# Kernel tuning notes

Measured on AMD Instinct MI355X. Metric: run time of the kernel, lower is better.

Reference implementation:

```python
import jax, jax.numpy as jnp
import numpy as np

P = 64        # patch size
NATOMS = 256  # dictionary atoms
N = 262144    # signal length
K = 262081    # npatches = N - P + 1 (stride-1 sliding patches)
M = 512       # measurement rows of A


def setup_inputs() -> dict:
    key = jax.random.key(0)
    k0, k1, k2, k3, k4, k5, k6 = jax.random.split(key, 7)
    d = jax.random.normal(k0, (1, P, NATOMS), jnp.float32) * 0.1
    x = jax.random.normal(k1, (NATOMS, K), jnp.float32) * 0.1
    ss = jnp.zeros((N, 1), jnp.float32)  # only its shape is used
    vb = (jax.random.uniform(k2, (N, 1)) > 0.05).astype(jnp.float32)
    # stride-1 sliding-window patch indices: column k covers [k, k+P)
    patches = (jnp.arange(K, dtype=jnp.int32)[None, :]
               + jnp.arange(P, dtype=jnp.int32)[:, None])  # [P, K]
    # npp = number of patches covering each signal sample
    npp = jnp.zeros((N, 1), jnp.float32).at[patches.reshape(-1), 0].add(1.0)
    sRef = jax.random.normal(k3, (N, 1), jnp.float32)
    A = jax.random.normal(k4, (M, N), jnp.float32) * 0.01
    Tarr = jax.random.normal(k5, (M, 1), jnp.float32)
    meanY = jnp.float32(0.1)
    ds = jax.random.normal(k6, (N, 1), jnp.float32)
    lam2 = jnp.float32(0.5)
    return {"d": d, "x": x, "ss": ss, "vb": vb, "patches": patches,
            "npp": npp, "sRef": sRef, "A": A, "Tarr": Tarr,
            "meanY": meanY, "ds": ds, "lam2": lam2, "npatches": K}


def reference(d, x, ss, vb, patches, npp, sRef, A, Tarr, meanY, ds, lam2, npatches):
    # ss_b[p, k] = (D @ X)[p, k] + meanY  -> per-patch reconstructions
    ss_b = jnp.squeeze(d) @ x + meanY                      # [P, K]
    # vectorized scatter-add replacing the torch loop over npatches
    ss_p_sum = jnp.zeros_like(ss).at[patches.reshape(-1), 0].add(ss_b.reshape(-1))  # [N,1]
    ss_f = (lam2 * ds + ss_p_sum) / (lam2 + npp)           # [N,1]
    ss_masked = ss_f * vb                                  # [N,1]
    Tref = A @ (ss_masked + sRef)                          # [M,1]
    return jnp.mean((Tref - Tarr) ** 2)
```

## Files before the change

### kernel.cpp

```cpp
#include <hip/hip_runtime.h>


namespace {
constexpr int kP = 64;
constexpr int kA = 256;
constexpr int kN = 262144;
constexpr int kK = 262081;
constexpr int kM = 512;

constexpr int CB = 256;
constexpr int OPT = 16;
constexpr int NB = CB * OPT;
constexpr int NCHUNK = kN / NB;
constexpr int NSPLIT = 16;
constexpr int APS = kA / NSPLIT;
constexpr int XS4 = 1088;
constexpr int DPF = 80;
constexpr int GV_CH = 8;

__device__ __forceinline__ int swz(int l4) { return l4 ^ ((l4 >> 3) & 7); }

__device__ __forceinline__ float f4c(const float4& v, int i) {
  switch (i & 3) {
    case 0: return v.x;
    case 1: return v.y;
    case 2: return v.z;
    default: return v.w;
  }
}

__device__ __forceinline__ void gload_lds16(const void* g, void* l) {
  __builtin_amdgcn_global_load_lds(
      (const __attribute__((address_space(1))) unsigned int*)g,
      (__attribute__((address_space(3))) unsigned int*)l, 16, 0, 0);
}

__device__ __forceinline__ void stage(const float* __restrict__ x, float4* buf,
                                      int a, int n0, int tid) {
  const int SA = (a + 1) & 3;
  const int g4base = (a * kK + n0 - 63 - SA) >> 2;
  const int g4max = (kA / 4) * kK - 1;
  const float4* __restrict__ x4 = (const float4*)x;
  const int wav = tid >> 6, lane = tid & 63;
  const int sl = lane ^ ((lane >> 3) & 7);
#pragma unroll
  for (int r = 0; r < 4; ++r) {
    const int s = r * 4 + wav;
    int g4 = g4base + s * 64 + sl;
    g4 = g4 < 0 ? 0 : (g4 > g4max ? g4max : g4);
    gload_lds16(x4 + g4, buf + s * 64);
  }
  if (tid < 20) {
    int g4 = g4base + 1024 + (tid ^ ((tid >> 3) & 7));
    g4 = g4 < 0 ? 0 : (g4 > g4max ? g4max : g4);
    gload_lds16(x4 + g4, buf + 1024);
  }
}

__device__ __forceinline__ void compute_atom(const float4* __restrict__ xs4,
                                             const float* __restrict__ dpf,
                                             int al, float* __restrict__ acc) {
  const int t4 = (int)threadIdx.x * 4;
  const float4* __restrict__ dp4 = (const float4*)(dpf + al * DPF);
  float4 w[5];
#pragma unroll
  for (int q = 0; q < 4; ++q) w[q] = xs4[swz(t4 + q)];
#pragma unroll
  for (int c = 0; c < 17; ++c) {
    w[(c + 4) % 5] = xs4[swz(t4 + c + 4)];
    float4 D = dp4[c];
#pragma unroll
    for (int i = 0; i < 4; ++i) {
      float coef = f4c(D, i);
#pragma unroll
      for (int j = 0; j < OPT; ++j) {
        int off = i + j;
        acc[j] = fmaf(coef, f4c(w[(c + (off >> 2)) % 5], off & 3), acc[j]);
      }
    }
  }
}

__global__ __launch_bounds__(CB, 4) void conv_kernel(const float* __restrict__ d,
                                                     const float* __restrict__ x,
                                                     float* __restrict__ part) {
  __shared__ float4 xsA[XS4];
  __shared__ float4 xsB[XS4];
  __shared__ float dpf[APS * DPF];
  const int n0 = blockIdx.x * NB;
  const int a0 = blockIdx.y * APS;
  const int tid = threadIdx.x;

  for (int idx = tid; idx < APS * DPF; idx += CB) {
    int al = idx / DPF, q = idx - al * DPF;
    int a = a0 + al, SA = (a + 1) & 3;
    float v = 0.0f;
    if (q >= SA && q < SA + 64) v = d[(63 + SA - q) * kA + a];
    dpf[idx] = v;
  }

  stage(x, xsA, a0, n0, tid);
  __syncthreads();

  float acc[OPT];
#pragma unroll
  for (int j = 0; j < OPT; ++j) acc[j] = 0.0f;

  const bool first = (blockIdx.x == 0);
  const bool last = (blockIdx.x == NCHUNK - 1);

#pragma unroll 1
  for (int al = 0; al < APS; ++al) {
    float4* cur = (al & 1) ? xsB : xsA;
    float4* nxt = (al & 1) ? xsA : xsB;
    const int a = a0 + al;
    if (first | last) {
      const int SA = (a + 1) & 3;
      float* curf = (float*)cur;
      if (first) {
        if (tid < 63 + SA) {
          int slot = swz(tid >> 2);
          curf[slot * 4 + (tid & 3)] = 0.0f;
        }
      } else {
        const int iK = kK - n0 + 63 + SA;
        for (int i = iK + tid; i < 4176; i += CB) {
          int slot = swz(i >> 2);
          curf[slot * 4 + (i & 3)] = 0.0f;
        }
      }
      __syncthreads();
    }
    if (al + 1 < APS) stage(x, nxt, a0 + al + 1, n0, tid);
    compute_atom(cur, dpf, al, acc);
    __syncthreads();
  }

  float4* outp = (float4*)(part + (size_t)blockIdx.y * kN + n0 + tid * OPT);
#pragma unroll
  for (int j = 0; j < 4; ++j)
    outp[j] = make_float4(acc[4 * j], acc[4 * j + 1], acc[4 * j + 2], acc[4 * j + 3]);
}

__global__ void vmask_kernel(const float* __restrict__ part, const float* __restrict__ ds,
                             const float* __restrict__ npp, const float* __restrict__ vb,
                             const float* __restrict__ sRef,
                             const float* __restrict__ pMeanY,
                             const float* __restrict__ pLam2, float* __restrict__ v) {
  const int i = blockIdx.x * blockDim.x + threadIdx.x;
  const float meanY = pMeanY[0];
  const float lam2 = pLam2[0];
  float4 s = make_float4(0.f, 0.f, 0.f, 0.f);
#pragma unroll
  for (int c = 0; c < NSPLIT; ++c) {
    float4 p = ((const float4*)(part + (size_t)c * kN))[i];
    s.x += p.x; s.y += p.y; s.z += p.z; s.w += p.w;
  }
  const float4 dd = ((const float4*)ds)[i];
  const float4 np = ((const float4*)npp)[i];
  const float4 vbv = ((const float4*)vb)[i];
  const float4 sr = ((const float4*)sRef)[i];
  float4 r;
  r.x = (lam2 * dd.x + s.x + meanY * np.x) / (lam2 + np.x) * vbv.x + sr.x;
  r.y = (lam2 * dd.y + s.y + meanY * np.y) / (lam2 + np.y) * vbv.y + sr.y;
  r.z = (lam2 * dd.z + s.z + meanY * np.z) / (lam2 + np.z) * vbv.z + sr.z;
  r.w = (lam2 * dd.w + s.w + meanY * np.w) / (lam2 + np.w) * vbv.w + sr.w;
  ((float4*)v)[i] = r;
}

__global__ __launch_bounds__(256) void gemv_kernel(const float* __restrict__ A,
                                                   const float* __restrict__ v,
                                                   float* __restrict__ Tp) {
  const int m = blockIdx.x >> 3;
  const int ch = blockIdx.x & (GV_CH - 1);
  const float4* __restrict__ A4 = (const float4*)(A + (size_t)m * kN);
  const float4* __restrict__ v4 = (const float4*)v;
  const int b0 = ch * (kN / 4 / GV_CH) + threadIdx.x;
  float s = 0.0f;
#pragma unroll 8
  for (int r = 0; r < 32; ++r) {
    float4 av = A4[b0 + r * 256];
    float4 vv = v4[b0 + r * 256];
    s = fmaf(av.x, vv.x, s);
    s = fmaf(av.y, vv.y, s);
    s = fmaf(av.z, vv.z, s);
    s = fmaf(av.w, vv.w, s);
  }
#pragma unroll
  for (int o = 32; o > 0; o >>= 1) s += __shfl_down(s, o, 64);
  __shared__ float red[4];
  if ((threadIdx.x & 63) == 0) red[threadIdx.x >> 6] = s;
  __syncthreads();
  if (threadIdx.x == 0) Tp[blockIdx.x] = red[0] + red[1] + red[2] + red[3];
}

__global__ void loss_kernel(const float* __restrict__ Tp, const float* __restrict__ Tarr,
                            float* __restrict__ out) {
  const int tid = threadIdx.x;
  float s = 0.0f;
  for (int m = tid; m < kM; m += 256) {
    float t = 0.0f;
#pragma unroll
    for (int c = 0; c < GV_CH; ++c) t += Tp[m * GV_CH + c];
    float df = t - Tarr[m];
    s = fmaf(df, df, s);
  }
#pragma unroll
  for (int o = 32; o > 0; o >>= 1) s += __shfl_down(s, o, 64);
  __shared__ float red[4];
  if ((tid & 63) == 0) red[tid >> 6] = s;
  __syncthreads();
  if (tid == 0) out[0] = (red[0] + red[1] + red[2] + red[3]) * (1.0f / kM);
}

}

extern "C" void kernel_launch(void* const* d_in, const int* in_sizes, int n_in,
                              void* d_out, int out_size, void* d_ws, size_t ws_size,
                              hipStream_t stream) {
  const float* d    = (const float*)d_in[0];
  const float* x    = (const float*)d_in[1];
  const float* vb   = (const float*)d_in[3];
  const float* npp  = (const float*)d_in[5];
  const float* sRef = (const float*)d_in[6];
  const float* A    = (const float*)d_in[7];
  const float* Tarr = (const float*)d_in[8];
  const float* pMeanY = (const float*)d_in[9];
  const float* ds   = (const float*)d_in[10];
  const float* pLam2 = (const float*)d_in[11];
  float* out = (float*)d_out;

  float* part = (float*)d_ws;
  float* v    = part + (size_t)NSPLIT * kN;
  float* Tp   = v + kN;

  conv_kernel<<<dim3(NCHUNK, NSPLIT), CB, 0, stream>>>(d, x, part);
  vmask_kernel<<<kN / 4 / 256, 256, 0, stream>>>(part, ds, npp, vb, sRef, pMeanY, pLam2, v);
  gemv_kernel<<<kM * GV_CH, 256, 0, stream>>>(A, v, Tp);
  loss_kernel<<<1, 256, 0, stream>>>(Tp, Tarr, out);
}
```

Before: 921.6 us.

## Replace LDS double-buffer DMA staging with register-prefetch single buffer, raise split

The x-tile staging changes from direct global-to-LDS loads into two alternating LDS buffers to a register prefetch of the next atom, written into a single LDS buffer between compute steps. Halving LDS use allows the occupancy hint to go from 4 to 6 blocks per CU, and the atom split doubles to 32 to give more blocks. The cost is extra registers, an additional barrier per atom, and twice as many partial-sum planes for the reduction kernel to read.

Result: slower. 1.853 ms (+101.1%).

```diff
diff --git a/kernel.cpp b/kernel.cpp
--- a/kernel.cpp
+++ b/kernel.cpp
@@ -12,7 +12,7 @@
 constexpr int OPT = 16;
 constexpr int NB = CB * OPT;
 constexpr int NCHUNK = kN / NB;
-constexpr int NSPLIT = 16;
+constexpr int NSPLIT = 32;
 constexpr int APS = kA / NSPLIT;
 constexpr int XS4 = 1088;
 constexpr int DPF = 80;
@@ -29,32 +29,33 @@
   }
 }
 
-__device__ __forceinline__ void gload_lds16(const void* g, void* l) {
-  __builtin_amdgcn_global_load_lds(
-      (const __attribute__((address_space(1))) unsigned int*)g,
-      (__attribute__((address_space(3))) unsigned int*)l, 16, 0, 0);
-}
-
-__device__ __forceinline__ void stage(const float* __restrict__ x, float4* buf,
-                                      int a, int n0, int tid) {
+__device__ __forceinline__ void load_regs(const float* __restrict__ x, int a, int n0,
+                                          int tid, float4 r[4], float4& rt) {
   const int SA = (a + 1) & 3;
   const int g4base = (a * kK + n0 - 63 - SA) >> 2;
   const int g4max = (kA / 4) * kK - 1;
   const float4* __restrict__ x4 = (const float4*)x;
-  const int wav = tid >> 6, lane = tid & 63;
-  const int sl = lane ^ ((lane >> 3) & 7);
-#pragma unroll
-  for (int r = 0; r < 4; ++r) {
-    const int s = r * 4 + wav;
-    int g4 = g4base + s * 64 + sl;
+#pragma unroll
+  for (int q = 0; q < 4; ++q) {
+    int g4 = g4base + q * 256 + tid;
     g4 = g4 < 0 ? 0 : (g4 > g4max ? g4max : g4);
-    gload_lds16(x4 + g4, buf + s * 64);
+    r[q] = x4[g4];
   }
   if (tid < 20) {
-    int g4 = g4base + 1024 + (tid ^ ((tid >> 3) & 7));
+    int g4 = g4base + 1024 + tid;
     g4 = g4 < 0 ? 0 : (g4 > g4max ? g4max : g4);
-    gload_lds16(x4 + g4, buf + 1024);
-  }
+    rt = x4[g4];
+  }
+}
+
+__device__ __forceinline__ void write_lds(float4* xs, int tid, const float4 r[4],
+                                          const float4& rt) {
+#pragma unroll
+  for (int q = 0; q < 4; ++q) {
+    const int l = q * 256 + tid;
+    xs[(l & ~63) | swz(l & 63)] = r[q];
+  }
+  if (tid < 20) xs[1024 + swz(tid)] = rt;
 }
 
 __device__ __forceinline__ void compute_atom(const float4* __restrict__ xs4,
@@ -81,11 +82,10 @@
   }
 }
 
-__global__ __launch_bounds__(CB, 4) void conv_kernel(const float* __restrict__ d,
+__global__ __launch_bounds__(CB, 6) void conv_kernel(const float* __restrict__ d,
                                                      const float* __restrict__ x,
                                                      float* __restrict__ part) {
-  __shared__ float4 xsA[XS4];
-  __shared__ float4 xsB[XS4];
+  __shared__ float4 xs[XS4];
   __shared__ float dpf[APS * DPF];
   const int n0 = blockIdx.x * NB;
   const int a0 = blockIdx.y * APS;
@@ -99,8 +99,12 @@
     dpf[idx] = v;
   }
 
-  stage(x, xsA, a0, n0, tid);
+  float4 r[4];
+  float4 rt = make_float4(0.f, 0.f, 0.f, 0.f);
+  load_regs(x, a0, n0, tid, r, rt);
+  write_lds(xs, tid, r, rt);
   __syncthreads();
+  load_regs(x, a0 + 1, n0, tid, r, rt);
 
   float acc[OPT];
 #pragma unroll
@@ -111,29 +115,31 @@
 
 #pragma unroll 1
   for (int al = 0; al < APS; ++al) {
-    float4* cur = (al & 1) ? xsB : xsA;
-    float4* nxt = (al & 1) ? xsA : xsB;
     const int a = a0 + al;
     if (first | last) {
       const int SA = (a + 1) & 3;
-      float* curf = (float*)cur;
+      float* xsf = (float*)xs;
       if (first) {
         if (tid < 63 + SA) {
           int slot = swz(tid >> 2);
-          curf[slot * 4 + (tid & 3)] = 0.0f;
+          xsf[slot * 4 + (tid & 3)] = 0.0f;
         }
       } else {
         const int iK = kK - n0 + 63 + SA;
         for (int i = iK + tid; i < 4176; i += CB) {
           int slot = swz(i >> 2);
-          curf[slot * 4 + (i & 3)] = 0.0f;
+          xsf[slot * 4 + (i & 3)] = 0.0f;
         }
       }
       __syncthreads();
     }
-    if (al + 1 < APS) stage(x, nxt, a0 + al + 1, n0, tid);
-    compute_atom(cur, dpf, al, acc);
-    __syncthreads();
+    compute_atom(xs, dpf, al, acc);
+    if (al + 1 < APS) {
+      __syncthreads();
+      write_lds(xs, tid, r, rt);
+      __syncthreads();
+      if (al + 2 < APS) load_regs(x, a0 + al + 2, n0, tid, r, rt);
+    }
   }
 
   float4* outp = (float4*)(part + (size_t)blockIdx.y * kN + n0 + tid * OPT);
```
